# Performance work log

Measured on AMD Instinct MI355X. Metric: run time of the kernel, lower is better.

Reference implementation:

```python
import jax, jax.numpy as jnp
import numpy as np
from jax import lax

B, L, D, H = 32, 512, 1024, 1024


def setup_inputs() -> dict:
    key = jax.random.key(0)
    kx, kw, kb = jax.random.split(key, 3)
    x = jax.random.normal(kx, (B, L, D), dtype=jnp.float32)
    # nn.Linear(D+H, 4H): weight (4H, D+H), bias (4H,), uniform(-1/sqrt(fan_in), 1/sqrt(fan_in))
    bound = 1.0 / np.sqrt(D + H)
    W = jax.random.uniform(kw, (4 * H, D + H), minval=-bound, maxval=bound, dtype=jnp.float32)
    b = jax.random.uniform(kb, (4 * H,), minval=-bound, maxval=bound, dtype=jnp.float32)
    return {"x": x, "W": W, "b": b}


def reference(x, W, b):
    Bsz, Lseq, Din = x.shape
    Hd = W.shape[0] // 4

    def step(carry, x_t):
        h, c = carry
        combined = jnp.concatenate([h, x_t], axis=-1)          # (B, H+D)
        gates = combined @ W.T + b                              # (B, 4H)
        f, i, o, c_tilde = jnp.split(gates, 4, axis=-1)
        c_new = jax.nn.sigmoid(f) * c + jax.nn.sigmoid(i) * jnp.tanh(c_tilde)
        h_new = jax.nn.sigmoid(o) * jnp.tanh(c_new)
        return (h_new, c_new), h_new

    h0 = jnp.zeros((Bsz, Hd), dtype=x.dtype)
    c0 = jnp.zeros((Bsz, Hd), dtype=x.dtype)
    xs = jnp.transpose(x, (1, 0, 2))                            # (L, B, D)
    _, hs = lax.scan(step, (h0, c0), xs)                        # hs: (L, B, H)
    return jnp.transpose(hs, (1, 0, 2))                         # (B, L, H)
```

## Files before the change

### kernel.cpp

```cpp
#include <hip/hip_runtime.h>
#include <hip/hip_fp16.h>

#define B_SZ 32
#define L_SZ 512
#define D_SZ 1024
#define H_SZ 1024
#define NG   4096
#define M_SZ 16384

typedef __attribute__((ext_vector_type(8))) short short8;
typedef __attribute__((ext_vector_type(4))) float f32x4;
typedef __attribute__((ext_vector_type(4))) unsigned u32x4;
typedef __attribute__((ext_vector_type(4))) unsigned short u16x4;

static const size_t GX_OFF  = 0;
static const size_t XB_OFF  = 134217728;
static const size_t WH_OFF  = 167772160;
static const size_t WX_OFF  = 176160768;
static const size_t HB_OFF  = 184549376;
static const size_t FLG_OFF = 184680448;

__device__ __forceinline__ unsigned short f2bf(float f) {
  union { float f; unsigned u; } v; v.f = f;
  unsigned r = v.u + 0x7fffu + ((v.u >> 16) & 1u);
  return (unsigned short)(r >> 16);
}

__device__ __forceinline__ void gload_lds16(const void* g, void* l) {
  __builtin_amdgcn_global_load_lds(
      (const __attribute__((address_space(1))) unsigned*)g,
      (__attribute__((address_space(3))) unsigned*)l, 16, 0, 0);
}


__global__ __launch_bounds__(256) void k_convert_w(const float* __restrict__ W,
                                                   unsigned short* __restrict__ Wh,
                                                   unsigned short* __restrict__ Wx) {
  int idx = blockIdx.x * 256 + threadIdx.x;
  f32x4 v = ((const f32x4*)W)[idx];
  u16x4 o;
#pragma unroll
  for (int e = 0; e < 4; ++e) o[e] = f2bf(v[e]);
  int n   = idx >> 9;
  int col = (idx & 511) * 4;
  if (col < 1024) *(u16x4*)(Wh + (size_t)n * 1024 + col)          = o;
  else            *(u16x4*)(Wx + (size_t)n * 1024 + (col - 1024)) = o;
}

__global__ __launch_bounds__(256) void k_convert_x(const float* __restrict__ x,
                                                   unsigned short* __restrict__ xb) {
  int idx = blockIdx.x * 256 + threadIdx.x;
  f32x4 v = ((const f32x4*)x)[idx];
  u16x4 o;
#pragma unroll
  for (int e = 0; e < 4; ++e) o[e] = f2bf(v[e]);
  ((u16x4*)xb)[idx] = o;
}

__global__ __launch_bounds__(256) void k_zero(unsigned* __restrict__ p, int n) {
  int i = blockIdx.x * 256 + threadIdx.x;
  if (i < n) p[i] = 0u;
}


__global__ __launch_bounds__(256) void k_xgemm(const unsigned short* __restrict__ A,
                                               const unsigned short* __restrict__ Bw,
                                               __half* __restrict__ C) {
  __shared__ unsigned short sA[128 * 64];
  __shared__ unsigned short sB[128 * 64];
  const int m0 = blockIdx.x * 128;
  const int n0 = blockIdx.y * 128;
  const int tid = threadIdx.x;
  const int lane = tid & 63;
  const int w = tid >> 6;
  const int wm = w >> 1, wn = w & 1;
  f32x4 acc[4][4] = {};
  for (int k0 = 0; k0 < 1024; k0 += 64) {
#pragma unroll
    for (int it = 0; it < 4; ++it) {
      int chunk = it * 256 + w * 64 + lane;
      int row = chunk >> 3, kc = chunk & 7;
      gload_lds16(A + (size_t)(m0 + row) * 1024 + k0 + kc * 8,
                  (char*)sA + (size_t)(it * 256 + w * 64) * 16);
      gload_lds16(Bw + (size_t)(n0 + row) * 1024 + k0 + kc * 8,
                  (char*)sB + (size_t)(it * 256 + w * 64) * 16);
    }
    asm volatile("s_waitcnt vmcnt(0)" ::: "memory");
    __syncthreads();
#pragma unroll
    for (int ks = 0; ks < 2; ++ks) {
      short8 af[4], bfr[4];
#pragma unroll
      for (int i = 0; i < 4; ++i) {
        int arow = wm * 64 + i * 16 + (lane & 15);
        af[i] = *(const short8*)(sA + arow * 64 + ks * 32 + (lane >> 4) * 8);
      }
#pragma unroll
      for (int j = 0; j < 4; ++j) {
        int brow = wn * 64 + j * 16 + (lane & 15);
        bfr[j] = *(const short8*)(sB + brow * 64 + ks * 32 + (lane >> 4) * 8);
      }
#pragma unroll
      for (int i = 0; i < 4; ++i)
#pragma unroll
        for (int j = 0; j < 4; ++j)
          acc[i][j] = __builtin_amdgcn_mfma_f32_16x16x32_bf16(af[i], bfr[j], acc[i][j], 0, 0, 0);
    }
    __syncthreads();
  }
#pragma unroll
  for (int i = 0; i < 4; ++i)
#pragma unroll
    for (int j = 0; j < 4; ++j)
#pragma unroll
      for (int q = 0; q < 4; ++q) {
        int row = m0 + wm * 64 + i * 16 + (lane >> 4) * 4 + q;
        int col = n0 + wn * 64 + j * 16 + (lane & 15);
        C[(size_t)row * NG + col] = __float2half(acc[i][j][q]);
      }
}


__global__ __launch_bounds__(256) void k_lstm(const unsigned short* __restrict__ Whg,
                                              const __half* __restrict__ Gx,
                                              const float* __restrict__ bias,
                                              unsigned short* __restrict__ hbuf,
                                              float* __restrict__ out,
                                              unsigned* __restrict__ flags) {
  extern __shared__ char lds[];
  char* w_base = lds;
  char* h_base = lds + 65536;
  float* gates_s = (float*)(lds + 131072);
  float* bias_s  = (float*)(lds + 131072 + 4224);
  float* c_s     = (float*)(lds + 131072 + 4224 + 128);
  unsigned short* hlds = (unsigned short*)(lds + 131072 + 4224 + 128 + 1024);

  const int tid = threadIdx.x;
  const int lane = tid & 63;
  const int w = tid >> 6;
  const int wg = blockIdx.x;
  const int j0 = wg * 8;

  for (int i = tid; i < 4096; i += 256) {
    int c = i >> 7, kc = i & 127;
    int n = (c >> 3) * 1024 + j0 + (c & 7);
    u32x4 v = *(const u32x4*)(Whg + (size_t)n * 1024 + kc * 8);
    *(u32x4*)(w_base + c * 2048 + ((kc * 16) ^ ((c & 7) << 4))) = v;
  }
  if (tid < 32) bias_s[tid] = bias[(tid >> 3) * 1024 + j0 + (tid & 7)];
  c_s[tid] = 0.f;
  __syncthreads();

  const int mt = w >> 1, nt = w & 1;
  const int arow = mt * 16 + (lane & 15);
  const int brow = nt * 16 + (lane & 15);
  const char* aBase = h_base + arow * 2048;
  const char* bBase = w_base + brow * 2048;
  const int kslot = (lane >> 4) * 16;
  const int aswz = (arow & 7) << 4;
  const int bswz = (brow & 7) << 4;
  const int b_ = tid >> 3, jj = tid & 7;
  const float rb0 = bias_s[jj], rb1 = bias_s[8 + jj];
  const float rb2 = bias_s[16 + jj], rb3 = bias_s[24 + jj];

  const unsigned* fp0 = flags + (size_t)(2 * tid) * 16;
  const unsigned* fp1 = flags + (size_t)(2 * tid + 1) * 16;

  for (int t = 0; t < 512; ++t) {
    const unsigned short* hin = hbuf + (size_t)(t & 1) * 32768;
    unsigned short* hout = hbuf + (size_t)((t + 1) & 1) * 32768;

    u32x4 h0,h1,h2,h3,h4,h5,h6,h7,h8,h9,h10,h11,h12,h13,h14,h15;
#define HLD(r, it) asm volatile("global_load_dwordx4 %0, %1, off sc0 sc1" \
      : "=v"(r) : "v"((const char*)hin + (size_t)((it) * 256 + tid) * 16) : "memory")
    HLD(h0,0); HLD(h1,1); HLD(h2,2); HLD(h3,3);
    HLD(h4,4); HLD(h5,5); HLD(h6,6); HLD(h7,7);
    HLD(h8,8); HLD(h9,9); HLD(h10,10); HLD(h11,11);
    HLD(h12,12); HLD(h13,13); HLD(h14,14); HLD(h15,15);
#undef HLD
    const char* gxp = (const char*)(Gx + ((size_t)(b_ * L_SZ + t)) * NG + j0 + jj);
    unsigned gxa, gxb, gxc, gxd;
    asm volatile("global_load_ushort %0, %1, off" : "=v"(gxa) : "v"(gxp)        : "memory");
    asm volatile("global_load_ushort %0, %1, off" : "=v"(gxb) : "v"(gxp + 2048) : "memory");
    asm volatile("global_load_ushort %0, %1, off" : "=v"(gxc) : "v"(gxp + 4096) : "memory");
    asm volatile("global_load_ushort %0, %1, off" : "=v"(gxd) : "v"(gxp + 6144) : "memory");

#define HWR(r, it) { int i_ = (it) * 256 + tid; int bb_ = i_ >> 7, kc_ = i_ & 127; \
      *(u32x4*)(h_base + bb_ * 2048 + ((kc_ * 16) ^ ((bb_ & 7) << 4))) = r; }
    asm volatile("s_waitcnt vmcnt(12)" ::: "memory");
    HWR(h0,0); HWR(h1,1); HWR(h2,2); HWR(h3,3);
    HWR(h4,4); HWR(h5,5); HWR(h6,6); HWR(h7,7);
    asm volatile("s_waitcnt vmcnt(4)" ::: "memory");
    HWR(h8,8); HWR(h9,9); HWR(h10,10); HWR(h11,11);
    HWR(h12,12); HWR(h13,13); HWR(h14,14); HWR(h15,15);
#undef HWR
    __syncthreads();

    f32x4 acc = {0.f, 0.f, 0.f, 0.f};
#pragma unroll
    for (int ks = 0; ks < 32; ++ks) {
      int kb = ks * 64 + kslot;
      short8 a  = *(const short8*)(aBase + (kb ^ aswz));
      short8 bv = *(const short8*)(bBase + (kb ^ bswz));
      acc = __builtin_amdgcn_mfma_f32_16x16x32_bf16(a, bv, acc, 0, 0, 0);
    }
    __syncthreads();
#pragma unroll
    for (int q = 0; q < 4; ++q)
      gates_s[(mt * 16 + (lane >> 4) * 4 + q) * 33 + nt * 16 + (lane & 15)] = acc[q];
    __syncthreads();

    asm volatile("s_waitcnt vmcnt(0)" ::: "memory");
    {
      float sf = gates_s[b_ * 33 + jj]      + __half2float(__ushort_as_half((unsigned short)gxa)) + rb0;
      float si = gates_s[b_ * 33 + 8 + jj]  + __half2float(__ushort_as_half((unsigned short)gxb)) + rb1;
      float so = gates_s[b_ * 33 + 16 + jj] + __half2float(__ushort_as_half((unsigned short)gxc)) + rb2;
      float sc = gates_s[b_ * 33 + 24 + jj] + __half2float(__ushort_as_half((unsigned short)gxd)) + rb3;
      float gf = 1.f / (1.f + expf(-sf));
      float gi = 1.f / (1.f + expf(-si));
      float go = 1.f / (1.f + expf(-so));
      float cn = gf * c_s[tid] + gi * tanhf(sc);
      float hn = go * tanhf(cn);
      c_s[tid] = cn;
      out[((size_t)b_ * L_SZ + t) * H_SZ + j0 + jj] = hn;
      hlds[b_ * 8 + jj] = f2bf(hn);
    }

    if (t < 511) {
      __syncthreads();
      if (tid < 32) {
        u32x4 v = *(u32x4*)(hlds + tid * 8);
        unsigned short* hp = hout + (size_t)tid * H_SZ + j0;
        asm volatile("global_store_dwordx4 %0, %1, off sc0 sc1"
                     :: "v"(hp), "v"(v) : "memory");
      }
      asm volatile("s_waitcnt vmcnt(0)" ::: "memory");
      __syncthreads();
      if (tid == 0) {
        unsigned fv = (unsigned)(t + 1);
        const unsigned* myf = flags + (size_t)wg * 16;
        asm volatile("global_store_dword %0, %1, off sc0 sc1"
                     :: "v"(myf), "v"(fv) : "memory");
      }
      if (tid < 64) {
        unsigned fa, fb;
        do {
          asm volatile("global_load_dword %0, %2, off sc0 sc1\n\t"
                       "global_load_dword %1, %3, off sc0 sc1\n\t"
                       "s_waitcnt vmcnt(0)"
                       : "=v"(fa), "=v"(fb) : "v"(fp0), "v"(fp1) : "memory");
        } while (!__all(fa > (unsigned)t && fb > (unsigned)t));
      }
      __syncthreads();
    }
  }
}


extern "C" void kernel_launch(void* const* d_in, const int* in_sizes, int n_in,
                              void* d_out, int out_size, void* d_ws, size_t ws_size,
                              hipStream_t stream) {
  const float* x = (const float*)d_in[0];
  const float* W = (const float*)d_in[1];
  const float* b = (const float*)d_in[2];
  char* ws = (char*)d_ws;
  __half* Gx           = (__half*)(ws + GX_OFF);
  unsigned short* xb   = (unsigned short*)(ws + XB_OFF);
  unsigned short* Wh   = (unsigned short*)(ws + WH_OFF);
  unsigned short* Wx   = (unsigned short*)(ws + WX_OFF);
  unsigned short* hbuf = (unsigned short*)(ws + HB_OFF);
  unsigned* flags      = (unsigned*)(ws + FLG_OFF);
  float* out = (float*)d_out;

  k_convert_w<<<8192, 256, 0, stream>>>(W, Wh, Wx);
  k_convert_x<<<16384, 256, 0, stream>>>(x, xb);
  k_zero<<<136, 256, 0, stream>>>((unsigned*)(ws + HB_OFF), (131072 + 8192) / 4);

  k_xgemm<<<dim3(128, 32), 256, 0, stream>>>(xb, Wx, Gx);

  hipFuncSetAttribute((const void*)k_lstm,
                      hipFuncAttributeMaxDynamicSharedMemorySize, 137472);
  k_lstm<<<128, 256, 137472, stream>>>(Wh, Gx, b, hbuf, out, flags);
}
```

Before: 2.413 ms.

## Keep recurrent weight fragments in registers and trim per-step sync in LSTM loop

Recurrent weight B-fragments now sit in VGPRs (32 short8 per lane) instead of LDS, which removes one LDS read per MFMA and halves the shared-memory footprint. The MFMA chain is split into two accumulators to shorten the dependency chain. The h loads drop the sc0 sc1 cache bypass in favour of an agent-scope acquire fence after the barrier, one __syncthreads is removed, and the output store is moved after the h publish so it overlaps the flag spin. The cost is heavy register pressure (launch_bounds 256,1), and correctness now depends on the fence making the other blocks' h writes visible to plain loads.

```diff
diff --git a/kernel.cpp b/kernel.cpp
--- a/kernel.cpp
+++ b/kernel.cpp
@@ -121,19 +121,18 @@
 }
 
 
-__global__ __launch_bounds__(256) void k_lstm(const unsigned short* __restrict__ Whg,
-                                              const __half* __restrict__ Gx,
-                                              const float* __restrict__ bias,
-                                              unsigned short* __restrict__ hbuf,
-                                              float* __restrict__ out,
-                                              unsigned* __restrict__ flags) {
+__global__ __launch_bounds__(256, 1) void k_lstm(const unsigned short* __restrict__ Whg,
+                                                 const __half* __restrict__ Gx,
+                                                 const float* __restrict__ bias,
+                                                 unsigned short* __restrict__ hbuf,
+                                                 float* __restrict__ out,
+                                                 unsigned* __restrict__ flags) {
   extern __shared__ char lds[];
-  char* w_base = lds;
-  char* h_base = lds + 65536;
-  float* gates_s = (float*)(lds + 131072);
-  float* bias_s  = (float*)(lds + 131072 + 4224);
-  float* c_s     = (float*)(lds + 131072 + 4224 + 128);
-  unsigned short* hlds = (unsigned short*)(lds + 131072 + 4224 + 128 + 1024);
+  char* h_base = lds;
+  float* gates_s = (float*)(lds + 65536);
+  float* bias_s  = (float*)(lds + 65536 + 4224);
+  float* c_s     = (float*)(lds + 65536 + 4224 + 128);
+  unsigned short* hlds = (unsigned short*)(lds + 65536 + 4224 + 128 + 1024);
 
   const int tid = threadIdx.x;
   const int lane = tid & 63;
@@ -141,25 +140,23 @@
   const int wg = blockIdx.x;
   const int j0 = wg * 8;
 
-  for (int i = tid; i < 4096; i += 256) {
-    int c = i >> 7, kc = i & 127;
-    int n = (c >> 3) * 1024 + j0 + (c & 7);
-    u32x4 v = *(const u32x4*)(Whg + (size_t)n * 1024 + kc * 8);
-    *(u32x4*)(w_base + c * 2048 + ((kc * 16) ^ ((c & 7) << 4))) = v;
-  }
+  const int mt = w >> 1, nt = w & 1;
+  const int arow = mt * 16 + (lane & 15);
+  const char* aBase = h_base + arow * 2048;
+  const int kslot = (lane >> 4) * 16;
+  const int aswz = (arow & 7) << 4;
+  const int b_ = tid >> 3, jj = tid & 7;
+
+  const int brow = nt * 16 + (lane & 15);
+  const unsigned short* wrow =
+      Whg + (size_t)((brow >> 3) * 1024 + j0 + (brow & 7)) * 1024 + (lane >> 4) * 8;
+  short8 bfrag[32];
+#pragma unroll
+  for (int ks = 0; ks < 32; ++ks) bfrag[ks] = *(const short8*)(wrow + ks * 32);
+
   if (tid < 32) bias_s[tid] = bias[(tid >> 3) * 1024 + j0 + (tid & 7)];
   c_s[tid] = 0.f;
   __syncthreads();
-
-  const int mt = w >> 1, nt = w & 1;
-  const int arow = mt * 16 + (lane & 15);
-  const int brow = nt * 16 + (lane & 15);
-  const char* aBase = h_base + arow * 2048;
-  const char* bBase = w_base + brow * 2048;
-  const int kslot = (lane >> 4) * 16;
-  const int aswz = (arow & 7) << 4;
-  const int bswz = (brow & 7) << 4;
-  const int b_ = tid >> 3, jj = tid & 7;
   const float rb0 = bias_s[jj], rb1 = bias_s[8 + jj];
   const float rb2 = bias_s[16 + jj], rb3 = bias_s[24 + jj];
 
@@ -171,7 +168,7 @@
     unsigned short* hout = hbuf + (size_t)((t + 1) & 1) * 32768;
 
     u32x4 h0,h1,h2,h3,h4,h5,h6,h7,h8,h9,h10,h11,h12,h13,h14,h15;
-#define HLD(r, it) asm volatile("global_load_dwordx4 %0, %1, off sc0 sc1" \
+#define HLD(r, it) asm volatile("global_load_dwordx4 %0, %1, off" \
       : "=v"(r) : "v"((const char*)hin + (size_t)((it) * 256 + tid) * 16) : "memory")
     HLD(h0,0); HLD(h1,1); HLD(h2,2); HLD(h3,3);
     HLD(h4,4); HLD(h5,5); HLD(h6,6); HLD(h7,7);
@@ -196,14 +193,15 @@
 #undef HWR
     __syncthreads();
 
-    f32x4 acc = {0.f, 0.f, 0.f, 0.f};
-#pragma unroll
-    for (int ks = 0; ks < 32; ++ks) {
-      int kb = ks * 64 + kslot;
-      short8 a  = *(const short8*)(aBase + (kb ^ aswz));
-      short8 bv = *(const short8*)(bBase + (kb ^ bswz));
-      acc = __builtin_amdgcn_mfma_f32_16x16x32_bf16(a, bv, acc, 0, 0, 0);
-    }
+    f32x4 acc0 = {0.f, 0.f, 0.f, 0.f}, acc1 = {0.f, 0.f, 0.f, 0.f};
+#pragma unroll
+    for (int ks = 0; ks < 32; ks += 2) {
+      short8 a0 = *(const short8*)(aBase + ((ks * 64 + kslot) ^ aswz));
+      short8 a1 = *(const short8*)(aBase + (((ks + 1) * 64 + kslot) ^ aswz));
+      acc0 = __builtin_amdgcn_mfma_f32_16x16x32_bf16(a0, bfrag[ks],     acc0, 0, 0, 0);
+      acc1 = __builtin_amdgcn_mfma_f32_16x16x32_bf16(a1, bfrag[ks + 1], acc1, 0, 0, 0);
+    }
+    f32x4 acc = acc0 + acc1;
     __syncthreads();
 #pragma unroll
     for (int q = 0; q < 4; ++q)
@@ -211,6 +209,7 @@
     __syncthreads();
 
     asm volatile("s_waitcnt vmcnt(0)" ::: "memory");
+    float hn;
     {
       float sf = gates_s[b_ * 33 + jj]      + __half2float(__ushort_as_half((unsigned short)gxa)) + rb0;
       float si = gates_s[b_ * 33 + 8 + jj]  + __half2float(__ushort_as_half((unsigned short)gxb)) + rb1;
@@ -220,11 +219,12 @@
       float gi = 1.f / (1.f + expf(-si));
       float go = 1.f / (1.f + expf(-so));
       float cn = gf * c_s[tid] + gi * tanhf(sc);
-      float hn = go * tanhf(cn);
+      hn = go * tanhf(cn);
       c_s[tid] = cn;
-      out[((size_t)b_ * L_SZ + t) * H_SZ + j0 + jj] = hn;
       hlds[b_ * 8 + jj] = f2bf(hn);
     }
+
+    float* outp = out + ((size_t)b_ * L_SZ + t) * H_SZ + j0 + jj;
 
     if (t < 511) {
       __syncthreads();
@@ -235,13 +235,14 @@
                      :: "v"(hp), "v"(v) : "memory");
       }
       asm volatile("s_waitcnt vmcnt(0)" ::: "memory");
-      __syncthreads();
       if (tid == 0) {
         unsigned fv = (unsigned)(t + 1);
         const unsigned* myf = flags + (size_t)wg * 16;
         asm volatile("global_store_dword %0, %1, off sc0 sc1"
                      :: "v"(myf), "v"(fv) : "memory");
       }
+      asm volatile("global_store_dword %0, %1, off sc0 sc1"
+                   :: "v"(outp), "v"(hn) : "memory");
       if (tid < 64) {
         unsigned fa, fb;
         do {
@@ -252,6 +253,10 @@
         } while (!__all(fa > (unsigned)t && fb > (unsigned)t));
       }
       __syncthreads();
+      __builtin_amdgcn_fence(__ATOMIC_ACQUIRE, "agent");
+    } else {
+      asm volatile("global_store_dword %0, %1, off sc0 sc1"
+                   :: "v"(outp), "v"(hn) : "memory");
     }
   }
 }
@@ -279,6 +284,6 @@
   k_xgemm<<<dim3(128, 32), 256, 0, stream>>>(xb, Wx, Gx);
 
   hipFuncSetAttribute((const void*)k_lstm,
-                      hipFuncAttributeMaxDynamicSharedMemorySize, 137472);
-  k_lstm<<<128, 256, 137472, stream>>>(Wh, Gx, b, hbuf, out, flags);
-}
+                      hipFuncAttributeMaxDynamicSharedMemorySize, 71424);
+  k_lstm<<<128, 256, 71424, stream>>>(Wh, Gx, b, hbuf, out, flags);
+}
```

After: 4.107 ms. 70.2% more time.

## Use write-once hidden-state ring buffer to allow cached loads in recurrence

Applied to the files above, without the earlier changes.

Replaces the double-buffered hidden-state exchange with a 512-slot ring that reuses the bf16 x workspace once the input GEMM has consumed it. Because each slot is written only once, the per-step h loads can drop the cache-bypass bits and use ordinary cached loads. The kernel also adds an agent-scope acquire fence at start, writes xb and the flags with write-through stores, and skips the h load at t=0. It further removes one block barrier and moves the output store after the flag publish, so it overlaps with the spin-wait. The risk is stale cache lines from the earlier xb use and weaker ordering between steps, which could break correctness.

```diff
diff --git a/kernel.cpp b/kernel.cpp
--- a/kernel.cpp
+++ b/kernel.cpp
@@ -17,7 +17,6 @@
 static const size_t XB_OFF  = 134217728;
 static const size_t WH_OFF  = 167772160;
 static const size_t WX_OFF  = 176160768;
-static const size_t HB_OFF  = 184549376;
 static const size_t FLG_OFF = 184680448;
 
 __device__ __forceinline__ unsigned short f2bf(float f) {
@@ -54,12 +53,19 @@
   u16x4 o;
 #pragma unroll
   for (int e = 0; e < 4; ++e) o[e] = f2bf(v[e]);
-  ((u16x4*)xb)[idx] = o;
-}
-
-__global__ __launch_bounds__(256) void k_zero(unsigned* __restrict__ p, int n) {
+  unsigned long long val;
+  __builtin_memcpy(&val, &o, 8);
+  unsigned short* p = xb + (size_t)idx * 4;
+  asm volatile("global_store_dwordx2 %0, %1, off sc0 sc1"
+               :: "v"(p), "v"(val) : "memory");
+}
+
+__global__ __launch_bounds__(256) void k_zero_wt(unsigned* __restrict__ p, int n) {
   int i = blockIdx.x * 256 + threadIdx.x;
-  if (i < n) p[i] = 0u;
+  unsigned z = 0u;
+  if (i < n)
+    asm volatile("global_store_dword %0, %1, off sc0 sc1"
+                 :: "v"(p + i), "v"(z) : "memory");
 }
 
 
@@ -124,7 +130,7 @@
 __global__ __launch_bounds__(256) void k_lstm(const unsigned short* __restrict__ Whg,
                                               const __half* __restrict__ Gx,
                                               const float* __restrict__ bias,
-                                              unsigned short* __restrict__ hbuf,
+                                              unsigned short* __restrict__ ring,
                                               float* __restrict__ out,
                                               unsigned* __restrict__ flags) {
   extern __shared__ char lds[];
@@ -140,6 +146,8 @@
   const int w = tid >> 6;
   const int wg = blockIdx.x;
   const int j0 = wg * 8;
+
+  __builtin_amdgcn_fence(__ATOMIC_ACQUIRE, "agent");
 
   for (int i = tid; i < 4096; i += 256) {
     int c = i >> 7, kc = i & 127;
@@ -167,17 +175,21 @@
   const unsigned* fp1 = flags + (size_t)(2 * tid + 1) * 16;
 
   for (int t = 0; t < 512; ++t) {
-    const unsigned short* hin = hbuf + (size_t)(t & 1) * 32768;
-    unsigned short* hout = hbuf + (size_t)((t + 1) & 1) * 32768;
-
-    u32x4 h0,h1,h2,h3,h4,h5,h6,h7,h8,h9,h10,h11,h12,h13,h14,h15;
-#define HLD(r, it) asm volatile("global_load_dwordx4 %0, %1, off sc0 sc1" \
+    const unsigned short* hin = ring + (size_t)t * 32768;
+    unsigned short* hout = (unsigned short*)ring + (size_t)(t + 1) * 32768;
+
+    u32x4 hz = {0u, 0u, 0u, 0u};
+    u32x4 h0=hz,h1=hz,h2=hz,h3=hz,h4=hz,h5=hz,h6=hz,h7=hz,
+          h8=hz,h9=hz,h10=hz,h11=hz,h12=hz,h13=hz,h14=hz,h15=hz;
+    if (t) {
+#define HLD(r, it) asm volatile("global_load_dwordx4 %0, %1, off" \
       : "=v"(r) : "v"((const char*)hin + (size_t)((it) * 256 + tid) * 16) : "memory")
-    HLD(h0,0); HLD(h1,1); HLD(h2,2); HLD(h3,3);
-    HLD(h4,4); HLD(h5,5); HLD(h6,6); HLD(h7,7);
-    HLD(h8,8); HLD(h9,9); HLD(h10,10); HLD(h11,11);
-    HLD(h12,12); HLD(h13,13); HLD(h14,14); HLD(h15,15);
+      HLD(h0,0); HLD(h1,1); HLD(h2,2); HLD(h3,3);
+      HLD(h4,4); HLD(h5,5); HLD(h6,6); HLD(h7,7);
+      HLD(h8,8); HLD(h9,9); HLD(h10,10); HLD(h11,11);
+      HLD(h12,12); HLD(h13,13); HLD(h14,14); HLD(h15,15);
 #undef HLD
+    }
     const char* gxp = (const char*)(Gx + ((size_t)(b_ * L_SZ + t)) * NG + j0 + jj);
     unsigned gxa, gxb, gxc, gxd;
     asm volatile("global_load_ushort %0, %1, off" : "=v"(gxa) : "v"(gxp)        : "memory");
@@ -211,6 +223,7 @@
     __syncthreads();
 
     asm volatile("s_waitcnt vmcnt(0)" ::: "memory");
+    float hn;
     {
       float sf = gates_s[b_ * 33 + jj]      + __half2float(__ushort_as_half((unsigned short)gxa)) + rb0;
       float si = gates_s[b_ * 33 + 8 + jj]  + __half2float(__ushort_as_half((unsigned short)gxb)) + rb1;
@@ -220,11 +233,11 @@
       float gi = 1.f / (1.f + expf(-si));
       float go = 1.f / (1.f + expf(-so));
       float cn = gf * c_s[tid] + gi * tanhf(sc);
-      float hn = go * tanhf(cn);
+      hn = go * tanhf(cn);
       c_s[tid] = cn;
-      out[((size_t)b_ * L_SZ + t) * H_SZ + j0 + jj] = hn;
       hlds[b_ * 8 + jj] = f2bf(hn);
     }
+    float* outp = out + ((size_t)b_ * L_SZ + t) * H_SZ + j0 + jj;
 
     if (t < 511) {
       __syncthreads();
@@ -235,13 +248,13 @@
                      :: "v"(hp), "v"(v) : "memory");
       }
       asm volatile("s_waitcnt vmcnt(0)" ::: "memory");
-      __syncthreads();
       if (tid == 0) {
         unsigned fv = (unsigned)(t + 1);
         const unsigned* myf = flags + (size_t)wg * 16;
         asm volatile("global_store_dword %0, %1, off sc0 sc1"
                      :: "v"(myf), "v"(fv) : "memory");
       }
+      *outp = hn;
       if (tid < 64) {
         unsigned fa, fb;
         do {
@@ -252,6 +265,8 @@
         } while (!__all(fa > (unsigned)t && fb > (unsigned)t));
       }
       __syncthreads();
+    } else {
+      *outp = hn;
     }
   }
 }
@@ -268,17 +283,16 @@
   unsigned short* xb   = (unsigned short*)(ws + XB_OFF);
   unsigned short* Wh   = (unsigned short*)(ws + WH_OFF);
   unsigned short* Wx   = (unsigned short*)(ws + WX_OFF);
-  unsigned short* hbuf = (unsigned short*)(ws + HB_OFF);
   unsigned* flags      = (unsigned*)(ws + FLG_OFF);
   float* out = (float*)d_out;
 
   k_convert_w<<<8192, 256, 0, stream>>>(W, Wh, Wx);
   k_convert_x<<<16384, 256, 0, stream>>>(x, xb);
-  k_zero<<<136, 256, 0, stream>>>((unsigned*)(ws + HB_OFF), (131072 + 8192) / 4);
+  k_zero_wt<<<8, 256, 0, stream>>>(flags, 8192 / 4);
 
   k_xgemm<<<dim3(128, 32), 256, 0, stream>>>(xb, Wx, Gx);
 
   hipFuncSetAttribute((const void*)k_lstm,
                       hipFuncAttributeMaxDynamicSharedMemorySize, 137472);
-  k_lstm<<<128, 256, 137472, stream>>>(Wh, Gx, b, hbuf, out, flags);
-}
+  k_lstm<<<128, 256, 137472, stream>>>(Wh, Gx, b, xb, out, flags);
+}
```

New measurement: 2.389 ms. Within noise of the previous version (-1.0%).
